# Kernel tuning notes

Measured on AMD Instinct MI355X. Metric: run time of the kernel, lower is better.

## Reference

```python
import jax, jax.numpy as jnp
import numpy as np

N, E, G, B = 50000, 1600000, 128, 128
FP = 33     # num_feature_pro
ED = 128    # embed_dim
ML = 3000   # max_len


def setup_inputs() -> dict:
    key = jax.random.key(0)
    ks = jax.random.split(key, 20)
    s = lambda k, shape: jax.random.normal(k, shape, jnp.float32) * 0.02
    inp = {}
    inp["pro_x"] = jax.random.normal(ks[0], (N, FP), jnp.float32)
    inp["edge_index"] = jax.random.randint(ks[1], (2, E), 0, N)
    inp["edge_weight"] = jax.random.uniform(ks[2], (E,), jnp.float32)
    inp["pro_batch"] = jnp.sort(jax.random.randint(ks[3], (N,), 0, G))
    inp["rna_global"] = jax.random.randint(ks[4], (B, ML), 0, 5)
    inp["rna_local"] = jax.random.randint(ks[5], (B, ML - 2), 0, 65)
    inp["emb1"] = s(ks[6], (5, ED))
    inp["emb2"] = s(ks[7], (65, ED))
    inp["convW1"] = s(ks[8], (32, ML, 8));     inp["convb1"] = jnp.zeros((32,), jnp.float32)
    inp["convW2"] = s(ks[9], (32, ML - 2, 8)); inp["convb2"] = jnp.zeros((32,), jnp.float32)
    inp["fcxr_W"] = s(ks[10], (32 * 121, 128)); inp["fcxr_b"] = jnp.zeros((128,), jnp.float32)
    inp["gcn1_W"] = s(ks[11], (FP, FP));         inp["gcn1_b"] = jnp.zeros((FP,), jnp.float32)
    inp["gcn2_W"] = s(ks[12], (FP, 2 * FP));     inp["gcn2_b"] = jnp.zeros((2 * FP,), jnp.float32)
    inp["gcn3_W"] = s(ks[13], (2 * FP, 4 * FP)); inp["gcn3_b"] = jnp.zeros((4 * FP,), jnp.float32)
    inp["bn1_g"] = jnp.ones((FP,), jnp.float32);     inp["bn1_b"] = jnp.zeros((FP,), jnp.float32)
    inp["bn2_g"] = jnp.ones((2 * FP,), jnp.float32); inp["bn2_b"] = jnp.zeros((2 * FP,), jnp.float32)
    inp["bn3_g"] = jnp.ones((4 * FP,), jnp.float32); inp["bn3_b"] = jnp.zeros((4 * FP,), jnp.float32)
    inp["fcg1_W"] = s(ks[14], (4 * FP, 1024)); inp["fcg1_b"] = jnp.zeros((1024,), jnp.float32)
    inp["fcg2_W"] = s(ks[15], (1024, 128));    inp["fcg2_b"] = jnp.zeros((128,), jnp.float32)
    return inp


def _gcn(x, W, b, src, dst, ew, n):
    # PyG GCNConv: x' = D^{-1/2}(A+I)D^{-1/2} (x W) + b, self-loop weight 1
    xw = x @ W                                           # [n, out]
    deg = jax.ops.segment_sum(ew, dst, num_segments=n) + 1.0
    dis = jax.lax.rsqrt(deg)
    norm = dis[src] * ew * dis[dst]                      # [E]
    out = jax.ops.segment_sum(xw[src] * norm[:, None], dst, num_segments=n)
    out = out + xw * (dis * dis)[:, None]                # self loops
    return out + b


def _bn(x, g, b, eps=1e-5):
    # NodeLevelBatchNorm (training): batch stats over the node dim, biased var
    m = x.mean(0)
    v = ((x - m) ** 2).mean(0)
    return (x - m) * jax.lax.rsqrt(v + eps) * g + b


def _conv1d(x, W, b):
    # x: [B, C, L], W: [O, C, K] -> [B, O, L-K+1]
    y = jax.lax.conv_general_dilated(x, W, (1,), 'VALID',
                                     dimension_numbers=('NCH', 'OIH', 'NCH'))
    return y + b[None, :, None]


def _rna(tok, emb, cW, cb, fW, fb):
    e = emb[tok]                     # [B, seq, 128] -> channels=seq, length=128
    y = _conv1d(e, cW, cb)           # [B, 32, 121]
    return y.reshape(y.shape[0], -1) @ fW + fb


def reference(pro_x, edge_index, edge_weight, pro_batch, rna_global, rna_local,
              emb1, emb2, convW1, convb1, convW2, convb2, fcxr_W, fcxr_b,
              gcn1_W, gcn1_b, gcn2_W, gcn2_b, gcn3_W, gcn3_b,
              bn1_g, bn1_b, bn2_g, bn2_b, bn3_g, bn3_b,
              fcg1_W, fcg1_b, fcg2_W, fcg2_b):
    src, dst = edge_index[0], edge_index[1]
    n = pro_x.shape[0]
    # RNA branch (fc_xr shared between global and local)
    xrg = _rna(rna_global, emb1, convW1, convb1, fcxr_W, fcxr_b)
    xrl = _rna(rna_local, emb2, convW2, convb2, fcxr_W, fcxr_b)
    # Protein GCN branch
    xp = jax.nn.relu(_bn(_gcn(pro_x, gcn1_W, gcn1_b, src, dst, edge_weight, n), bn1_g, bn1_b))
    ones = jnp.ones_like(edge_weight)
    xp = jax.nn.relu(_bn(_gcn(xp, gcn2_W, gcn2_b, src, dst, ones, n), bn2_g, bn2_b))
    xp = jax.nn.relu(_bn(_gcn(xp, gcn3_W, gcn3_b, src, dst, ones, n), bn3_g, bn3_b))
    # global mean pool per graph
    cnt = jax.ops.segment_sum(jnp.ones((n,), xp.dtype), pro_batch, num_segments=G)
    pooled = jax.ops.segment_sum(xp, pro_batch, num_segments=G) / jnp.maximum(cnt, 1.0)[:, None]
    h = jax.nn.relu(pooled @ fcg1_W + fcg1_b)
    xp_out = h @ fcg2_W + fcg2_b     # dropout = identity (eval)
    xc_rna = (xrg + xrl) * 0.5       # mean over stacked [xrg, xrl]
    return (xc_rna, xp_out)
```

## Files before the change

kernel.cpp:

```cpp
#include <hip/hip_runtime.h>
#include <hip/hip_bf16.h>

typedef __hip_bfloat16 bf16;

#define NN 50000
#define NE 1600000
#define NG 128
#define NB 128
#define SG 3000
#define SL 2998
#define VG 5
#define VL 65
#define EDB 6250
#define AGB 12500
#define NA  (NB*VG + NB*VL)
#define NGB (32*VG + 32*VL)
#define CASTB ((NN*40+255)/256)

__device__ __forceinline__ float b2f(bf16 x){ return __bfloat162float(x); }
__device__ __forceinline__ float blo(unsigned u){ return __uint_as_float(u << 16); }
__device__ __forceinline__ float bhi(unsigned u){ return __uint_as_float(u & 0xffff0000u); }

__global__ void k_front(const int* __restrict__ rna_g, const int* __restrict__ rna_l,
                        int* __restrict__ tcnt_g, int* __restrict__ toff_g,
                        int* __restrict__ bucket_g,
                        int* __restrict__ tcnt_l, int* __restrict__ toff_l,
                        int* __restrict__ bucket_l,
                        const float* __restrict__ convW1, const float* __restrict__ convW2,
                        float* __restrict__ Wr1, float* __restrict__ Wr2,
                        const float* __restrict__ fcxrW, const float* __restrict__ cb1,
                        const float* __restrict__ cb2, float* __restrict__ bias0,
                        const int* __restrict__ dst, const float* __restrict__ ew,
                        double* __restrict__ packed, int* __restrict__ slot){
    int bx = blockIdx.x;
    int t = threadIdx.x;
    if (bx < 2*NB){
        __shared__ int hist[VL], pre[VL], cur[VL];
        int br = bx & 1, b = bx >> 1;
        const int* tok = br ? rna_l : rna_g;
        int S = br ? SL : SG, V = br ? VL : VG;
        int* tcnt = br ? tcnt_l : tcnt_g;
        int* toff = br ? toff_l : toff_g;
        int* bucket = br ? bucket_l : bucket_g;
        if (t < V) hist[t] = 0;
        __syncthreads();
        for (int i = t; i < S; i += 256) atomicAdd(&hist[tok[b*S + i]], 1);
        __syncthreads();
        if (t == 0){
            int run = 0;
            for (int v = 0; v < V; ++v){ pre[v] = run; run += hist[v]; }
        }
        __syncthreads();
        if (t < V){
            tcnt[b*V + t] = hist[t];
            toff[b*V + t] = pre[t];
            cur[t] = pre[t];
        }
        __syncthreads();
        for (int i = t; i < S; i += 256){
            int v = tok[b*S + i];
            int p = atomicAdd(&cur[v], 1);
            bucket[b*S + p] = i;
        }
        return;
    }
    bx -= 2*NB;
    if (bx < EDB){
        int e = bx*256 + t;
        double old = unsafeAtomicAdd(&packed[dst[e]], 1048576.0 + (double)ew[e]);
        slot[e] = (int)(old * (1.0/1048576.0));
        return;
    }
    bx -= EDB;
    if (bx < SG + SL){
        const float* W; float* Wr; int S, c = bx;
        if (c < SG){ W = convW1; Wr = Wr1; S = SG; }
        else { c -= SG; W = convW2; Wr = Wr2; S = SL; }
        Wr[c*256 + t] = W[((t >> 3)*S + c)*8 + (t & 7)];
        return;
    }
    bx -= SG + SL;
    if (t >= 128) return;
    int o = bx, j = t;
    float s = 0.f;
    const float* Wo = fcxrW + o*121*128 + j;
    for (int l = 0; l < 121; ++l) s += Wo[l*128];
    unsafeAtomicAdd(&bias0[j], 0.5f * (cb1[o] + cb2[o]) * s);
}

__device__ void dev_buildA(const float* __restrict__ Wr, const int* __restrict__ bucket,
                           const int* __restrict__ toff, const int* __restrict__ tcnt,
                           float* __restrict__ A, int S, int V, int bv){
    int b = bv / V, v = bv - b*V;
    int t = threadIdx.x;
    const int* bk = bucket + b*S + toff[b*V + v];
    int m = tcnt[b*V + v];
    float acc = 0.f;
    int idx = 0;
    for (; idx + 4 <= m; idx += 4){
        int c0 = bk[idx], c1 = bk[idx+1], c2 = bk[idx+2], c3 = bk[idx+3];
        acc += Wr[c0*256 + t];
        acc += Wr[c1*256 + t];
        acc += Wr[c2*256 + t];
        acc += Wr[c3*256 + t];
    }
    for (; idx < m; ++idx) acc += Wr[bk[idx]*256 + t];
    A[b*(256*V) + v*256 + t] = acc;
}

__global__ void k_F1(const float* __restrict__ Wr1, const float* __restrict__ Wr2,
                     const int* __restrict__ bucket_g, const int* __restrict__ toff_g,
                     const int* __restrict__ tcnt_g, float* __restrict__ Ag,
                     const int* __restrict__ bucket_l, const int* __restrict__ toff_l,
                     const int* __restrict__ tcnt_l, float* __restrict__ Al,
                     const double* __restrict__ packed, int* __restrict__ cnt,
                     float2* __restrict__ dis12, float2* __restrict__ self12,
                     const int* __restrict__ batch, int* __restrict__ gstart,
                     int* __restrict__ bsum,
                     const float* __restrict__ fcxrb, const float* __restrict__ bias0,
                     float* __restrict__ out0){
    __shared__ int sd[256];
    int bx = blockIdx.x;
    if (bx < NA){
        if (bx < NB*VG) dev_buildA(Wr1, bucket_g, toff_g, tcnt_g, Ag, SG, VG, bx);
        else dev_buildA(Wr2, bucket_l, toff_l, tcnt_l, Al, SL, VL, bx - NB*VG);
        return;
    }
    bx -= NA;
    int t = threadIdx.x;
    if (bx == 49){
        for (int idx = t; idx < NB*128; idx += 256)
            out0[idx] = fcxrb[idx & 127] + bias0[idx & 127];
        return;
    }
    int base = bx*1024;
    int s = 0;
    #pragma unroll
    for (int j = 0; j < 4; ++j){
        int i = base + t*4 + j;
        if (i < NN){
            double p = packed[i];
            int c = (int)(p * (1.0/1048576.0));
            float w = (float)(p - (double)c * 1048576.0);
            cnt[i] = c; s += c;
            float r1 = rsqrtf(w + 1.0f);
            float r2 = rsqrtf((float)c + 1.0f);
            dis12[i] = make_float2(r1, r2);
            self12[i] = make_float2(r1*r1, r2*r2);
            int pb = batch[i];
            int prev = (i == 0) ? -1 : batch[i-1];
            for (int g = prev + 1; g <= pb; ++g) gstart[g] = i;
            if (i == NN - 1){
                for (int g = pb + 1; g <= NG; ++g) gstart[g] = NN;
            }
        }
    }
    sd[t] = s; __syncthreads();
    for (int d = 128; d > 0; d >>= 1){
        if (t < d) sd[t] += sd[t+d];
        __syncthreads();
    }
    if (t == 0) bsum[bx] = sd[0];
}

__global__ void k_scan3(const int* __restrict__ cnt, const int* __restrict__ bsum,
                        int* __restrict__ offs){
    __shared__ int sd[256];
    __shared__ int sbase;
    int t = threadIdx.x;
    if (t == 0){
        int run = 0;
        for (int i = 0; i < blockIdx.x; ++i) run += bsum[i];
        sbase = run;
    }
    int base = blockIdx.x*1024;
    int loc[4]; int s = 0;
    #pragma unroll
    for (int j = 0; j < 4; ++j){
        int idx = base + t*4 + j;
        loc[j] = (idx < NN) ? cnt[idx] : 0;
        s += loc[j];
    }
    sd[t] = s; __syncthreads();
    for (int d = 1; d < 256; d <<= 1){
        int v = (t >= d) ? sd[t-d] : 0;
        __syncthreads();
        sd[t] += v;
        __syncthreads();
    }
    int run = sbase + (sd[t] - s);
    #pragma unroll
    for (int j = 0; j < 4; ++j){
        int idx = base + t*4 + j;
        if (idx < NN) offs[idx] = run;
        run += loc[j];
    }
}

__device__ void dev_buildG(float (*rows)[128], const float* __restrict__ emb,
                           const float* __restrict__ W, bf16* __restrict__ G,
                           int V, int q){
    int o = q / V, mt = q - o*V;
    int t = threadIdx.x;
    int j = t & 127, half = t >> 7;
    int kk[4], vv[4];
    #pragma unroll
    for (int qq = 0; qq < 4; ++qq){
        int mm = half*4 + qq;
        int m = mt*8 + mm;
        int k = m / V, v = m - k*V;
        kk[qq] = k; vv[qq] = v;
        rows[mm][j] = emb[v*128 + j];
    }
    __syncthreads();
    float a0=0.f, a1=0.f, a2=0.f, a3=0.f;
    const float* Wo = W + o*121*128 + j;
    for (int l = 0; l < 121; ++l){
        float w = Wo[l*128];
        a0 += rows[half*4+0][l + kk[0]] * w;
        a1 += rows[half*4+1][l + kk[1]] * w;
        a2 += rows[half*4+2][l + kk[2]] * w;
        a3 += rows[half*4+3][l + kk[3]] * w;
    }
    float a[4] = {a0, a1, a2, a3};
    #pragma unroll
    for (int qq = 0; qq < 4; ++qq){
        int row = vv[qq]*256 + o*8 + kk[qq];
        G[(size_t)row*128 + j] = __float2bfloat16(a[qq]);
    }
}

__global__ void k_F2(const int* __restrict__ src, const int* __restrict__ dst,
                     const float* __restrict__ ew, const float2* __restrict__ dis12,
                     const int* __restrict__ offs, const int* __restrict__ slot,
                     float4* __restrict__ epk,
                     const float* __restrict__ emb1, const float* __restrict__ emb2,
                     const float* __restrict__ fcxrW, bf16* __restrict__ G1,
                     bf16* __restrict__ G2,
                     const float* __restrict__ pro_x, bf16* __restrict__ xb0){
    __shared__ float rows[8][128];
    int bx = blockIdx.x;
    if (bx < 32*VG){ dev_buildG(rows, emb1, fcxrW, G1, VG, bx); return; }
    if (bx < NGB){ dev_buildG(rows, emb2, fcxrW, G2, VL, bx - 32*VG); return; }
    bx -= NGB;
    if (bx < EDB){
        int e = bx*256 + threadIdx.x;
        int s = src[e], d = dst[e];
        int pos = offs[d] + slot[e];
        float2 a = dis12[s], b = dis12[d];
        float4 v;
        v.x = __int_as_float(s*80);
        v.y = a.x * ew[e] * b.x;
        v.z = a.y * b.y;
        v.w = __int_as_float(s*144);
        epk[pos] = v;
        return;
    }
    bx -= EDB;
    int i = bx*256 + threadIdx.x;
    if (i >= NN*40) return;
    int n = i / 40, f = i - n*40;
    xb0[i] = __float2bfloat16(f < 33 ? pro_x[n*33 + f] : 0.f);
}

template<int QV, int GRP, int OFF_W, int N_Z>
__device__ void dev_agg(float* sAgg ,
                        const bf16* __restrict__ xb, const float4* __restrict__ epk,
                        const int* __restrict__ offs, const int* __restrict__ cnt,
                        const float2* __restrict__ self12,
                        const float* __restrict__ W, const float* __restrict__ bias,
                        float* __restrict__ tout, float* __restrict__ bnpart,
                        int F, int OF, int bx){
    const int LPG = 64 / GRP;
    int wave = threadIdx.x >> 6;
    int node = bx*4 + wave;
    int lane = threadIdx.x & 63;
    int grp  = lane / LPG;
    int gl   = lane % LPG;
    bool act = gl < QV;
    const char* xc = (const char*)xb;
    float a0=0,a1=0,a2=0,a3=0,a4=0,a5=0,a6=0,a7=0;
    int b = offs[node], e = b + cnt[node];
    if (act){
        int fo = gl << 4;
        if (grp == 0){
            float2 sw2 = self12[node];
            float sw = N_Z ? sw2.y : sw2.x;
            uint4 u = *(const uint4*)(xc + node*(QV*16) + fo);
            a0 = sw*blo(u.x); a1 = sw*bhi(u.x); a2 = sw*blo(u.y); a3 = sw*bhi(u.y);
            a4 = sw*blo(u.z); a5 = sw*bhi(u.z); a6 = sw*blo(u.w); a7 = sw*bhi(u.w);
        }
        int p = b + grp;
        for (; p + 3*GRP < e; p += 4*GRP){
            float4 e0 = epk[p];
            float4 e1 = epk[p +   GRP];
            float4 e2 = epk[p + 2*GRP];
            float4 e3 = epk[p + 3*GRP];
            int o0 = __float_as_int(OFF_W ? e0.w : e0.x); float n0 = N_Z ? e0.z : e0.y;
            int o1 = __float_as_int(OFF_W ? e1.w : e1.x); float n1 = N_Z ? e1.z : e1.y;
            int o2 = __float_as_int(OFF_W ? e2.w : e2.x); float n2 = N_Z ? e2.z : e2.y;
            int o3 = __float_as_int(OFF_W ? e3.w : e3.x); float n3 = N_Z ? e3.z : e3.y;
            uint4 u0 = *(const uint4*)(xc + o0 + fo);
            uint4 u1 = *(const uint4*)(xc + o1 + fo);
            uint4 u2 = *(const uint4*)(xc + o2 + fo);
            uint4 u3 = *(const uint4*)(xc + o3 + fo);
            a0 += n0*blo(u0.x); a1 += n0*bhi(u0.x); a2 += n0*blo(u0.y); a3 += n0*bhi(u0.y);
            a4 += n0*blo(u0.z); a5 += n0*bhi(u0.z); a6 += n0*blo(u0.w); a7 += n0*bhi(u0.w);
            a0 += n1*blo(u1.x); a1 += n1*bhi(u1.x); a2 += n1*blo(u1.y); a3 += n1*bhi(u1.y);
            a4 += n1*blo(u1.z); a5 += n1*bhi(u1.z); a6 += n1*blo(u1.w); a7 += n1*bhi(u1.w);
            a0 += n2*blo(u2.x); a1 += n2*bhi(u2.x); a2 += n2*blo(u2.y); a3 += n2*bhi(u2.y);
            a4 += n2*blo(u2.z); a5 += n2*bhi(u2.z); a6 += n2*blo(u2.w); a7 += n2*bhi(u2.w);
            a0 += n3*blo(u3.x); a1 += n3*bhi(u3.x); a2 += n3*blo(u3.y); a3 += n3*bhi(u3.y);
            a4 += n3*blo(u3.z); a5 += n3*bhi(u3.z); a6 += n3*blo(u3.w); a7 += n3*bhi(u3.w);
        }
        if (p < e){
            int p1 = p + GRP, p2 = p + 2*GRP;
            bool v1 = p1 < e, v2 = p2 < e;
            float4 e0 = epk[p];
            float4 e1 = epk[v1 ? p1 : p];
            float4 e2 = epk[v2 ? p2 : p];
            int o0 = __float_as_int(OFF_W ? e0.w : e0.x);
            int o1 = __float_as_int(OFF_W ? e1.w : e1.x);
            int o2 = __float_as_int(OFF_W ? e2.w : e2.x);
            float n0 = N_Z ? e0.z : e0.y;
            float n1 = v1 ? (N_Z ? e1.z : e1.y) : 0.f;
            float n2 = v2 ? (N_Z ? e2.z : e2.y) : 0.f;
            uint4 u0 = *(const uint4*)(xc + o0 + fo);
            uint4 u1 = *(const uint4*)(xc + o1 + fo);
            uint4 u2 = *(const uint4*)(xc + o2 + fo);
            a0 += n0*blo(u0.x); a1 += n0*bhi(u0.x); a2 += n0*blo(u0.y); a3 += n0*bhi(u0.y);
            a4 += n0*blo(u0.z); a5 += n0*bhi(u0.z); a6 += n0*blo(u0.w); a7 += n0*bhi(u0.w);
            a0 += n1*blo(u1.x); a1 += n1*bhi(u1.x); a2 += n1*blo(u1.y); a3 += n1*bhi(u1.y);
            a4 += n1*blo(u1.z); a5 += n1*bhi(u1.z); a6 += n1*blo(u1.w); a7 += n1*bhi(u1.w);
            a0 += n2*blo(u2.x); a1 += n2*bhi(u2.x); a2 += n2*blo(u2.y); a3 += n2*bhi(u2.y);
            a4 += n2*blo(u2.z); a5 += n2*bhi(u2.z); a6 += n2*blo(u2.w); a7 += n2*bhi(u2.w);
        }
    }
    #pragma unroll
    for (int m = LPG; m < 64; m <<= 1){
        a0 += __shfl_xor(a0, m); a1 += __shfl_xor(a1, m);
        a2 += __shfl_xor(a2, m); a3 += __shfl_xor(a3, m);
        a4 += __shfl_xor(a4, m); a5 += __shfl_xor(a5, m);
        a6 += __shfl_xor(a6, m); a7 += __shfl_xor(a7, m);
    }
    if (act && grp == 0){
        float4* dst = (float4*)&sAgg[wave*(QV*8) + gl*8];
        dst[0] = make_float4(a0, a1, a2, a3);
        dst[1] = make_float4(a4, a5, a6, a7);
    }
    __syncthreads();
    int i0 = bx*4;
    int j = threadIdx.x;
    if (j < OF){
        float c0 = bias[j], c1 = c0, c2 = c0, c3 = c0;
        const float* Wj = W + j;
        const float* s0 = sAgg;
        const float* s1 = sAgg + QV*8;
        const float* s2 = sAgg + 2*QV*8;
        const float* s3 = sAgg + 3*QV*8;
        #pragma unroll 4
        for (int f = 0; f < F; ++f){
            float w = Wj[f*OF];
            c0 += s0[f]*w; c1 += s1[f]*w; c2 += s2[f]*w; c3 += s3[f]*w;
        }
        tout[(size_t)(i0+0)*OF + j] = c0;
        tout[(size_t)(i0+1)*OF + j] = c1;
        tout[(size_t)(i0+2)*OF + j] = c2;
        tout[(size_t)(i0+3)*OF + j] = c3;
        float s  = c0 + c1 + c2 + c3;
        float ss = c0*c0 + c1*c1 + c2*c2 + c3*c3;
        float* part = bnpart + (bx & 63)*(2*OF);
        unsafeAtomicAdd(&part[j], s);
        unsafeAtomicAdd(&part[OF + j], ss);
    }
}

template<int QV, int GRP, int OFF_W, int N_Z>
__global__ void k_agg_gemm(const bf16* __restrict__ xb, const float4* __restrict__ epk,
                           const int* __restrict__ offs, const int* __restrict__ cnt,
                           const float2* __restrict__ self12,
                           const float* __restrict__ W, const float* __restrict__ bias,
                           float* __restrict__ tout, float* __restrict__ bnpart,
                           int F, int OF){
    __shared__ float sAgg[4*QV*8];
    dev_agg<QV,GRP,OFF_W,N_Z>(sAgg, xb, epk, offs, cnt, self12, W, bias,
                              tout, bnpart, F, OF, blockIdx.x);
}

__device__ void dev_gemmR(float* xs , int bq,
                          const float* __restrict__ Ag, const bf16* __restrict__ G1,
                          const float* __restrict__ Al, const bf16* __restrict__ G2,
                          float* __restrict__ out0){
    int kpart = bq >> 4;
    int bgrp  = bq & 15;
    const float* X; const bf16* G; int K, k0;
    if (kpart < 5){ X = Ag; G = G1; K = 1280;  k0 = kpart*256; }
    else          { X = Al; G = G2; K = 16640; k0 = (kpart-5)*256; }
    int b0 = bgrp*8;
    int t = threadIdx.x;
    #pragma unroll
    for (int i = 0; i < 8; ++i)
        xs[i*256 + t] = X[(b0+i)*K + k0 + t];
    __syncthreads();
    int rq = t >> 7, j = t & 127;
    const float* x0 = xs + (rq*4)*256;
    float a0=0,a1=0,a2=0,a3=0;
    const bf16* Gp = G + (size_t)k0*128 + j;
    for (int kk = 0; kk < 256; ++kk){
        float g = b2f(Gp[kk*128]);
        a0 += x0[kk]*g; a1 += x0[256+kk]*g; a2 += x0[512+kk]*g; a3 += x0[768+kk]*g;
    }
    unsafeAtomicAdd(&out0[(b0+rq*4+0)*128 + j], 0.5f*a0);
    unsafeAtomicAdd(&out0[(b0+rq*4+1)*128 + j], 0.5f*a1);
    unsafeAtomicAdd(&out0[(b0+rq*4+2)*128 + j], 0.5f*a2);
    unsafeAtomicAdd(&out0[(b0+rq*4+3)*128 + j], 0.5f*a3);
}

__global__ void k_L3(const bf16* __restrict__ xb, const float4* __restrict__ epk,
                     const int* __restrict__ offs, const int* __restrict__ cnt,
                     const float2* __restrict__ self12,
                     const float* __restrict__ W, const float* __restrict__ bias,
                     float* __restrict__ tout, float* __restrict__ bnpart,
                     const float* __restrict__ Ag, const bf16* __restrict__ G1,
                     const float* __restrict__ Al, const bf16* __restrict__ G2,
                     float* __restrict__ out0){
    __shared__ float smem[8*256];
    int bx = blockIdx.x;
    if (bx < AGB){
        dev_agg<9,4,1,1>(smem, xb, epk, offs, cnt, self12, W, bias, tout, bnpart,
                         66, 132, bx);
    } else {
        dev_gemmR(smem, bx - AGB, Ag, G1, Al, G2, out0);
    }
}

__global__ void k_bn_fin(const float* __restrict__ part, float* __restrict__ sums, int OF){
    int tid = threadIdx.x;
    if (tid >= 2*OF) return;
    float s = 0.f;
    #pragma unroll 8
    for (int k = 0; k < 64; ++k) s += part[k*(2*OF) + tid];
    sums[tid] = s;
}

__global__ void k_bn_apply(const float* __restrict__ t, const float* __restrict__ sums,
                           const float* __restrict__ g, const float* __restrict__ b,
                           bf16* __restrict__ xo, int OF, int OS, int total){
    int id = blockIdx.x*256 + threadIdx.x;
    if (id >= total) return;
    int i = id / OS, f = id - i*OS;
    float v = 0.f;
    if (f < OF){
        float m  = sums[f] * (1.0f/(float)NN);
        float vr = sums[OF + f] * (1.0f/(float)NN) - m*m;
        float sc = g[f] * rsqrtf(vr + 1e-5f);
        float sh = b[f] - m*sc;
        v = t[(size_t)i*OF + f] * sc + sh;
        v = v > 0.f ? v : 0.f;
    }
    xo[id] = __float2bfloat16(v);
}

__global__ void k_poolBN(const float* __restrict__ t, const float* __restrict__ sums,
                         const float* __restrict__ g, const float* __restrict__ b,
                         const int* __restrict__ gstart, float* __restrict__ poolsum){
    int gr = blockIdx.x, strip = blockIdx.y, f = threadIdx.x;
    if (f >= 132) return;
    float m  = sums[f] * (1.0f/(float)NN);
    float vr = sums[132 + f] * (1.0f/(float)NN) - m*m;
    float sc = g[f] * rsqrtf(vr + 1e-5f);
    float sh = b[f] - m*sc;
    int i0 = gstart[gr], i1 = gstart[gr+1];
    float s = 0.f;
    for (int i = i0 + strip; i < i1; i += 4){
        float v = t[(size_t)i*132 + f] * sc + sh;
        s += v > 0.f ? v : 0.f;
    }
    unsafeAtomicAdd(&poolsum[gr*132 + f], s);
}

__global__ void k_fcgF(const float* __restrict__ poolsum, const int* __restrict__ gstart,
                       const float* __restrict__ W1, const float* __restrict__ b1,
                       const float* __restrict__ W2, const float* __restrict__ b2,
                       float* __restrict__ out){
    __shared__ float pr[132];
    __shared__ float hr[1024];
    __shared__ float part[8][128];
    int g = blockIdx.x, t = threadIdx.x;
    if (t < 132){
        float inv = 1.0f / fmaxf((float)(gstart[g+1] - gstart[g]), 1.0f);
        pr[t] = poolsum[g*132 + t] * inv;
    }
    __syncthreads();
    float acc = b1[t];
    #pragma unroll 4
    for (int f = 0; f < 132; ++f) acc += pr[f] * W1[f*1024 + t];
    hr[t] = acc > 0.f ? acc : 0.f;
    __syncthreads();
    int ks = t >> 7, j = t & 127;
    const float* Wp = W2 + (ks*128)*128 + j;
    const float* hp = hr + ks*128;
    float a = 0.f;
    #pragma unroll 8
    for (int kk = 0; kk < 128; ++kk) a += hp[kk] * Wp[(size_t)kk*128];
    part[ks][j] = a;
    __syncthreads();
    if (t < 128){
        float s = b2[t];
        #pragma unroll
        for (int r = 0; r < 8; ++r) s += part[r][t];
        out[g*128 + t] = s;
    }
}

extern "C" void kernel_launch(void* const* d_in, const int* in_sizes, int n_in,
                              void* d_out, int out_size, void* d_ws, size_t ws_size,
                              hipStream_t stream)
{
    (void)in_sizes; (void)n_in; (void)out_size; (void)ws_size;

    const float* pro_x  = (const float*)d_in[0];
    const int*   eidx   = (const int*)  d_in[1];
    const float* ew     = (const float*)d_in[2];
    const int*   pbatch = (const int*)  d_in[3];
    const int*   rna_g  = (const int*)  d_in[4];
    const int*   rna_l  = (const int*)  d_in[5];
    const float* emb1   = (const float*)d_in[6];
    const float* emb2   = (const float*)d_in[7];
    const float* convW1 = (const float*)d_in[8];
    const float* convb1 = (const float*)d_in[9];
    const float* convW2 = (const float*)d_in[10];
    const float* convb2 = (const float*)d_in[11];
    const float* fcxrW  = (const float*)d_in[12];
    const float* fcxrb  = (const float*)d_in[13];
    const float* g1W = (const float*)d_in[14];
    const float* g1b = (const float*)d_in[15];
    const float* g2W = (const float*)d_in[16];
    const float* g2b = (const float*)d_in[17];
    const float* g3W = (const float*)d_in[18];
    const float* g3b = (const float*)d_in[19];
    const float* bn1g = (const float*)d_in[20];
    const float* bn1b = (const float*)d_in[21];
    const float* bn2g = (const float*)d_in[22];
    const float* bn2b = (const float*)d_in[23];
    const float* bn3g = (const float*)d_in[24];
    const float* bn3b = (const float*)d_in[25];
    const float* fcg1W = (const float*)d_in[26];
    const float* fcg1b = (const float*)d_in[27];
    const float* fcg2W = (const float*)d_in[28];
    const float* fcg2b = (const float*)d_in[29];

    const int* e_src = eidx;
    const int* e_dst = eidx + NE;

    char* base = (char*)d_ws;
    size_t off = 0;
    auto alloc = [&](size_t bytes)->char*{
        off = (off + 255) & ~(size_t)255;
        char* p = base + off; off += bytes; return p;
    };

    double* packed  = (double*)alloc(NN*8);
    float* bnsum1  = (float*)alloc(2*33*4);
    float* bnsum2  = (float*)alloc(2*66*4);
    float* bnsum3  = (float*)alloc(2*132*4);
    float* poolsum = (float*)alloc(NG*132*4);
    float* bias0   = (float*)alloc(128*4);
    float* bnpart1 = (float*)alloc(64*2*33*4);
    float* bnpart2 = (float*)alloc(64*2*66*4);
    float* bnpart3 = (float*)alloc(64*2*132*4);
    size_t zero_bytes = (off + 255) & ~(size_t)255;

    int*    cnt    = (int*)   alloc(NN*4);
    float2* dis12  = (float2*)alloc(NN*8);
    float2* self12 = (float2*)alloc(NN*8);
    int*    offs   = (int*)   alloc(NN*4);
    int*    bsum   = (int*)   alloc(64*4);
    int*    gstart = (int*)   alloc((NG+1)*4);
    float4* epk    = (float4*)alloc((size_t)NE*16);
    float*  bufB   = (float*) alloc((size_t)NN*132*4);
    bf16*   xbA    = (bf16*)  alloc((size_t)NE*4);
    bf16*   xbB    = (bf16*)  alloc((size_t)NN*72*2);
    float*  Ag     = (float*) alloc((size_t)NB*256*VG*4);
    float*  Al     = (float*) alloc((size_t)NB*256*VL*4);
    bf16*   G1     = (bf16*)  alloc((size_t)32*8*VG*128*2);
    bf16*   G2     = (bf16*)  alloc((size_t)32*8*VL*128*2);

    int*  slot = (int*)xbA;
    bf16* xb0  = (bf16*)xbB;

    float* out0 = (float*)d_out;
    float* out1 = (float*)d_out + 16384;

    char* rb = (char*)bufB;
    size_t ro = 0;
    auto ralloc = [&](size_t bytes)->char*{
        ro = (ro + 255) & ~(size_t)255;
        char* p = rb + ro; ro += bytes; return p;
    };
    int* toff_g   = (int*)ralloc(NB*VG*4);
    int* toff_l   = (int*)ralloc(NB*VL*4);
    int* tcnt_g   = (int*)ralloc(NB*VG*4);
    int* tcnt_l   = (int*)ralloc(NB*VL*4);
    int* bucket_g = (int*)ralloc((size_t)NB*SG*4);
    int* bucket_l = (int*)ralloc((size_t)NB*SL*4);
    float* Wr1    = (float*)ralloc((size_t)SG*256*4);
    float* Wr2    = (float*)ralloc((size_t)SL*256*4);

    hipMemsetAsync(d_ws, 0, zero_bytes, stream);

    k_front<<<2*NB + EDB + SG + SL + 32, 256, 0, stream>>>(
        rna_g, rna_l, tcnt_g, toff_g, bucket_g, tcnt_l, toff_l, bucket_l,
        convW1, convW2, Wr1, Wr2, fcxrW, convb1, convb2, bias0,
        e_dst, ew, packed, slot);

    k_F1<<<NA + 50, 256, 0, stream>>>(Wr1, Wr2,
                                      bucket_g, toff_g, tcnt_g, Ag,
                                      bucket_l, toff_l, tcnt_l, Al,
                                      packed, cnt, dis12, self12, pbatch, gstart,
                                      bsum, fcxrb, bias0, out0);
    k_scan3<<<49, 256, 0, stream>>>(cnt, bsum, offs);

    k_F2<<<NGB + EDB + CASTB, 256, 0, stream>>>(
        e_src, e_dst, ew, dis12, offs, slot, epk,
        emb1, emb2, fcxrW, G1, G2, pro_x, xb0);

    k_agg_gemm<5,8,0,0><<<AGB, 256, 0, stream>>>(xb0, epk, offs, cnt, self12,
                                                 g1W, g1b, bufB, bnpart1, 33, 33);
    k_bn_fin<<<1, 512, 0, stream>>>(bnpart1, bnsum1, 33);
    k_bn_apply<<<(NN*40+255)/256, 256, 0, stream>>>(bufB, bnsum1, bn1g, bn1b,
                                                    xbA, 33, 40, NN*40);

    k_agg_gemm<5,8,0,1><<<AGB, 256, 0, stream>>>(xbA, epk, offs, cnt, self12,
                                                 g2W, g2b, bufB, bnpart2, 33, 66);
    k_bn_fin<<<1, 512, 0, stream>>>(bnpart2, bnsum2, 66);
    k_bn_apply<<<(NN*72+255)/256, 256, 0, stream>>>(bufB, bnsum2, bn2g, bn2b,
                                                    xbB, 66, 72, NN*72);

    k_L3<<<AGB + 1120, 256, 0, stream>>>(xbB, epk, offs, cnt, self12,
                                         g3W, g3b, bufB, bnpart3, Ag, G1, Al, G2, out0);
    k_bn_fin<<<1, 512, 0, stream>>>(bnpart3, bnsum3, 132);

    k_poolBN<<<dim3(NG,4), 192, 0, stream>>>(bufB, bnsum3, bn3g, bn3b, gstart, poolsum);
    k_fcgF<<<NG, 1024, 0, stream>>>(poolsum, gstart, fcg1W, fcg1b, fcg2W, fcg2b, out1);
}
```

Before: 571.5 us.

## Remap GCN gather lanes to power-of-two slots with tail chunk handled by lane zero

Restructures the edge-gather aggregation so each wave splits into 64/MAIN edge slots of MAIN lanes (4 or 8) instead of groups with idle lanes (QV=5 or 9 in groups of 8 or 16 lanes). The leftover 16-byte feature chunk per row is handled by lane 0 of each slot with a second accumulator set. This packs more edges per wave and removes masked-off lanes. It also lowers unroll depth from 4 to 2 and adds launch bounds for 8 blocks per CU. The extra divergent lane-0 loads and doubled shuffle reductions add cost and create load imbalance within each slot.

Result: slower. 604.6 us (+5.8%).

```diff
diff --git a/kernel.cpp b/kernel.cpp
--- a/kernel.cpp
+++ b/kernel.cpp
@@ -263,7 +263,7 @@
     xb0[i] = __float2bfloat16(f < 33 ? pro_x[n*33 + f] : 0.f);
 }
 
-template<int QV, int GRP, int OFF_W, int N_Z>
+template<int MAIN, int OFF_W, int N_Z>
 __device__ void dev_agg(float* sAgg ,
                         const bf16* __restrict__ xb, const float4* __restrict__ epk,
                         const int* __restrict__ offs, const int* __restrict__ cnt,
@@ -271,82 +271,86 @@
                         const float* __restrict__ W, const float* __restrict__ bias,
                         float* __restrict__ tout, float* __restrict__ bnpart,
                         int F, int OF, int bx){
-    const int LPG = 64 / GRP;
+    const int NS  = 64 / MAIN;
+    const int ROW = (MAIN + 1) * 16;
+    const int PW  = (MAIN + 1) * 8;
     int wave = threadIdx.x >> 6;
     int node = bx*4 + wave;
     int lane = threadIdx.x & 63;
-    int grp  = lane / LPG;
-    int gl   = lane % LPG;
-    bool act = gl < QV;
+    int slot = lane / MAIN;
+    int gl   = lane & (MAIN - 1);
     const char* xc = (const char*)xb;
+    int fo = gl << 4;
+    const int fe = MAIN << 4;
     float a0=0,a1=0,a2=0,a3=0,a4=0,a5=0,a6=0,a7=0;
-    int b = offs[node], e = b + cnt[node];
-    if (act){
-        int fo = gl << 4;
-        if (grp == 0){
-            float2 sw2 = self12[node];
-            float sw = N_Z ? sw2.y : sw2.x;
-            uint4 u = *(const uint4*)(xc + node*(QV*16) + fo);
-            a0 = sw*blo(u.x); a1 = sw*bhi(u.x); a2 = sw*blo(u.y); a3 = sw*bhi(u.y);
-            a4 = sw*blo(u.z); a5 = sw*bhi(u.z); a6 = sw*blo(u.w); a7 = sw*bhi(u.w);
-        }
-        int p = b + grp;
-        for (; p + 3*GRP < e; p += 4*GRP){
-            float4 e0 = epk[p];
-            float4 e1 = epk[p +   GRP];
-            float4 e2 = epk[p + 2*GRP];
-            float4 e3 = epk[p + 3*GRP];
-            int o0 = __float_as_int(OFF_W ? e0.w : e0.x); float n0 = N_Z ? e0.z : e0.y;
-            int o1 = __float_as_int(OFF_W ? e1.w : e1.x); float n1 = N_Z ? e1.z : e1.y;
-            int o2 = __float_as_int(OFF_W ? e2.w : e2.x); float n2 = N_Z ? e2.z : e2.y;
-            int o3 = __float_as_int(OFF_W ? e3.w : e3.x); float n3 = N_Z ? e3.z : e3.y;
-            uint4 u0 = *(const uint4*)(xc + o0 + fo);
-            uint4 u1 = *(const uint4*)(xc + o1 + fo);
-            uint4 u2 = *(const uint4*)(xc + o2 + fo);
-            uint4 u3 = *(const uint4*)(xc + o3 + fo);
-            a0 += n0*blo(u0.x); a1 += n0*bhi(u0.x); a2 += n0*blo(u0.y); a3 += n0*bhi(u0.y);
-            a4 += n0*blo(u0.z); a5 += n0*bhi(u0.z); a6 += n0*blo(u0.w); a7 += n0*bhi(u0.w);
-            a0 += n1*blo(u1.x); a1 += n1*bhi(u1.x); a2 += n1*blo(u1.y); a3 += n1*bhi(u1.y);
-            a4 += n1*blo(u1.z); a5 += n1*bhi(u1.z); a6 += n1*blo(u1.w); a7 += n1*bhi(u1.w);
-            a0 += n2*blo(u2.x); a1 += n2*bhi(u2.x); a2 += n2*blo(u2.y); a3 += n2*bhi(u2.y);
-            a4 += n2*blo(u2.z); a5 += n2*bhi(u2.z); a6 += n2*blo(u2.w); a7 += n2*bhi(u2.w);
-            a0 += n3*blo(u3.x); a1 += n3*bhi(u3.x); a2 += n3*blo(u3.y); a3 += n3*bhi(u3.y);
-            a4 += n3*blo(u3.z); a5 += n3*bhi(u3.z); a6 += n3*blo(u3.w); a7 += n3*bhi(u3.w);
-        }
-        if (p < e){
-            int p1 = p + GRP, p2 = p + 2*GRP;
-            bool v1 = p1 < e, v2 = p2 < e;
-            float4 e0 = epk[p];
-            float4 e1 = epk[v1 ? p1 : p];
-            float4 e2 = epk[v2 ? p2 : p];
-            int o0 = __float_as_int(OFF_W ? e0.w : e0.x);
-            int o1 = __float_as_int(OFF_W ? e1.w : e1.x);
-            int o2 = __float_as_int(OFF_W ? e2.w : e2.x);
-            float n0 = N_Z ? e0.z : e0.y;
-            float n1 = v1 ? (N_Z ? e1.z : e1.y) : 0.f;
-            float n2 = v2 ? (N_Z ? e2.z : e2.y) : 0.f;
-            uint4 u0 = *(const uint4*)(xc + o0 + fo);
-            uint4 u1 = *(const uint4*)(xc + o1 + fo);
-            uint4 u2 = *(const uint4*)(xc + o2 + fo);
-            a0 += n0*blo(u0.x); a1 += n0*bhi(u0.x); a2 += n0*blo(u0.y); a3 += n0*bhi(u0.y);
-            a4 += n0*blo(u0.z); a5 += n0*bhi(u0.z); a6 += n0*blo(u0.w); a7 += n0*bhi(u0.w);
-            a0 += n1*blo(u1.x); a1 += n1*bhi(u1.x); a2 += n1*blo(u1.y); a3 += n1*bhi(u1.y);
-            a4 += n1*blo(u1.z); a5 += n1*bhi(u1.z); a6 += n1*blo(u1.w); a7 += n1*bhi(u1.w);
-            a0 += n2*blo(u2.x); a1 += n2*bhi(u2.x); a2 += n2*blo(u2.y); a3 += n2*bhi(u2.y);
-            a4 += n2*blo(u2.z); a5 += n2*bhi(u2.z); a6 += n2*blo(u2.w); a7 += n2*bhi(u2.w);
+    float b0=0,b1=0,b2=0,b3=0,b4=0,b5=0,b6=0,b7=0;
+    int bg = offs[node], e = bg + cnt[node];
+    if (slot == 0){
+        float2 sw2 = self12[node];
+        float sw = N_Z ? sw2.y : sw2.x;
+        const char* rp = xc + (size_t)node*ROW;
+        uint4 u = *(const uint4*)(rp + fo);
+        a0 = sw*blo(u.x); a1 = sw*bhi(u.x); a2 = sw*blo(u.y); a3 = sw*bhi(u.y);
+        a4 = sw*blo(u.z); a5 = sw*bhi(u.z); a6 = sw*blo(u.w); a7 = sw*bhi(u.w);
+        if (gl == 0){
+            uint4 v = *(const uint4*)(rp + fe);
+            b0 = sw*blo(v.x); b1 = sw*bhi(v.x); b2 = sw*blo(v.y); b3 = sw*bhi(v.y);
+            b4 = sw*blo(v.z); b5 = sw*bhi(v.z); b6 = sw*blo(v.w); b7 = sw*bhi(v.w);
+        }
+    }
+    int p = bg + slot;
+    for (; p + NS < e; p += 2*NS){
+        float4 e0 = epk[p];
+        float4 e1 = epk[p + NS];
+        int o0 = __float_as_int(OFF_W ? e0.w : e0.x); float n0 = N_Z ? e0.z : e0.y;
+        int o1 = __float_as_int(OFF_W ? e1.w : e1.x); float n1 = N_Z ? e1.z : e1.y;
+        uint4 u0 = *(const uint4*)(xc + o0 + fo);
+        uint4 u1 = *(const uint4*)(xc + o1 + fo);
+        a0 += n0*blo(u0.x); a1 += n0*bhi(u0.x); a2 += n0*blo(u0.y); a3 += n0*bhi(u0.y);
+        a4 += n0*blo(u0.z); a5 += n0*bhi(u0.z); a6 += n0*blo(u0.w); a7 += n0*bhi(u0.w);
+        a0 += n1*blo(u1.x); a1 += n1*bhi(u1.x); a2 += n1*blo(u1.y); a3 += n1*bhi(u1.y);
+        a4 += n1*blo(u1.z); a5 += n1*bhi(u1.z); a6 += n1*blo(u1.w); a7 += n1*bhi(u1.w);
+        if (gl == 0){
+            uint4 v0 = *(const uint4*)(xc + o0 + fe);
+            uint4 v1 = *(const uint4*)(xc + o1 + fe);
+            b0 += n0*blo(v0.x); b1 += n0*bhi(v0.x); b2 += n0*blo(v0.y); b3 += n0*bhi(v0.y);
+            b4 += n0*blo(v0.z); b5 += n0*bhi(v0.z); b6 += n0*blo(v0.w); b7 += n0*bhi(v0.w);
+            b0 += n1*blo(v1.x); b1 += n1*bhi(v1.x); b2 += n1*blo(v1.y); b3 += n1*bhi(v1.y);
+            b4 += n1*blo(v1.z); b5 += n1*bhi(v1.z); b6 += n1*blo(v1.w); b7 += n1*bhi(v1.w);
+        }
+    }
+    if (p < e){
+        float4 e0 = epk[p];
+        int o0 = __float_as_int(OFF_W ? e0.w : e0.x); float n0 = N_Z ? e0.z : e0.y;
+        uint4 u0 = *(const uint4*)(xc + o0 + fo);
+        a0 += n0*blo(u0.x); a1 += n0*bhi(u0.x); a2 += n0*blo(u0.y); a3 += n0*bhi(u0.y);
+        a4 += n0*blo(u0.z); a5 += n0*bhi(u0.z); a6 += n0*blo(u0.w); a7 += n0*bhi(u0.w);
+        if (gl == 0){
+            uint4 v0 = *(const uint4*)(xc + o0 + fe);
+            b0 += n0*blo(v0.x); b1 += n0*bhi(v0.x); b2 += n0*blo(v0.y); b3 += n0*bhi(v0.y);
+            b4 += n0*blo(v0.z); b5 += n0*bhi(v0.z); b6 += n0*blo(v0.w); b7 += n0*bhi(v0.w);
         }
     }
     #pragma unroll
-    for (int m = LPG; m < 64; m <<= 1){
+    for (int m = MAIN; m < 64; m <<= 1){
         a0 += __shfl_xor(a0, m); a1 += __shfl_xor(a1, m);
         a2 += __shfl_xor(a2, m); a3 += __shfl_xor(a3, m);
         a4 += __shfl_xor(a4, m); a5 += __shfl_xor(a5, m);
         a6 += __shfl_xor(a6, m); a7 += __shfl_xor(a7, m);
-    }
-    if (act && grp == 0){
-        float4* dst = (float4*)&sAgg[wave*(QV*8) + gl*8];
-        dst[0] = make_float4(a0, a1, a2, a3);
-        dst[1] = make_float4(a4, a5, a6, a7);
+        b0 += __shfl_xor(b0, m); b1 += __shfl_xor(b1, m);
+        b2 += __shfl_xor(b2, m); b3 += __shfl_xor(b3, m);
+        b4 += __shfl_xor(b4, m); b5 += __shfl_xor(b5, m);
+        b6 += __shfl_xor(b6, m); b7 += __shfl_xor(b7, m);
+    }
+    if (slot == 0){
+        float4* d = (float4*)&sAgg[wave*PW + gl*8];
+        d[0] = make_float4(a0, a1, a2, a3);
+        d[1] = make_float4(a4, a5, a6, a7);
+        if (gl == 0){
+            float4* d2 = (float4*)&sAgg[wave*PW + MAIN*8];
+            d2[0] = make_float4(b0, b1, b2, b3);
+            d2[1] = make_float4(b4, b5, b6, b7);
+        }
     }
     __syncthreads();
     int i0 = bx*4;
@@ -355,9 +359,9 @@
         float c0 = bias[j], c1 = c0, c2 = c0, c3 = c0;
         const float* Wj = W + j;
         const float* s0 = sAgg;
-        const float* s1 = sAgg + QV*8;
-        const float* s2 = sAgg + 2*QV*8;
-        const float* s3 = sAgg + 3*QV*8;
+        const float* s1 = sAgg + PW;
+        const float* s2 = sAgg + 2*PW;
+        const float* s3 = sAgg + 3*PW;
         #pragma unroll 4
         for (int f = 0; f < F; ++f){
             float w = Wj[f*OF];
@@ -375,16 +379,17 @@
     }
 }
 
-template<int QV, int GRP, int OFF_W, int N_Z>
-__global__ void k_agg_gemm(const bf16* __restrict__ xb, const float4* __restrict__ epk,
-                           const int* __restrict__ offs, const int* __restrict__ cnt,
-                           const float2* __restrict__ self12,
-                           const float* __restrict__ W, const float* __restrict__ bias,
-                           float* __restrict__ tout, float* __restrict__ bnpart,
-                           int F, int OF){
-    __shared__ float sAgg[4*QV*8];
-    dev_agg<QV,GRP,OFF_W,N_Z>(sAgg, xb, epk, offs, cnt, self12, W, bias,
-                              tout, bnpart, F, OF, blockIdx.x);
+template<int MAIN, int OFF_W, int N_Z>
+__global__ __launch_bounds__(256, 8)
+void k_agg_gemm(const bf16* __restrict__ xb, const float4* __restrict__ epk,
+                const int* __restrict__ offs, const int* __restrict__ cnt,
+                const float2* __restrict__ self12,
+                const float* __restrict__ W, const float* __restrict__ bias,
+                float* __restrict__ tout, float* __restrict__ bnpart,
+                int F, int OF){
+    __shared__ float sAgg[4*(MAIN+1)*8];
+    dev_agg<MAIN,OFF_W,N_Z>(sAgg, xb, epk, offs, cnt, self12, W, bias,
+                            tout, bnpart, F, OF, blockIdx.x);
 }
 
 __device__ void dev_gemmR(float* xs , int bq,
@@ -416,19 +421,20 @@
     unsafeAtomicAdd(&out0[(b0+rq*4+3)*128 + j], 0.5f*a3);
 }
 
-__global__ void k_L3(const bf16* __restrict__ xb, const float4* __restrict__ epk,
-                     const int* __restrict__ offs, const int* __restrict__ cnt,
-                     const float2* __restrict__ self12,
-                     const float* __restrict__ W, const float* __restrict__ bias,
-                     float* __restrict__ tout, float* __restrict__ bnpart,
-                     const float* __restrict__ Ag, const bf16* __restrict__ G1,
-                     const float* __restrict__ Al, const bf16* __restrict__ G2,
-                     float* __restrict__ out0){
+__global__ __launch_bounds__(256, 8)
+void k_L3(const bf16* __restrict__ xb, const float4* __restrict__ epk,
+          const int* __restrict__ offs, const int* __restrict__ cnt,
+          const float2* __restrict__ self12,
+          const float* __restrict__ W, const float* __restrict__ bias,
+          float* __restrict__ tout, float* __restrict__ bnpart,
+          const float* __restrict__ Ag, const bf16* __restrict__ G1,
+          const float* __restrict__ Al, const bf16* __restrict__ G2,
+          float* __restrict__ out0){
     __shared__ float smem[8*256];
     int bx = blockIdx.x;
     if (bx < AGB){
-        dev_agg<9,4,1,1>(smem, xb, epk, offs, cnt, self12, W, bias, tout, bnpart,
-                         66, 132, bx);
+        dev_agg<8,1,1>(smem, xb, epk, offs, cnt, self12, W, bias, tout, bnpart,
+                       66, 132, bx);
     } else {
         dev_gemmR(smem, bx - AGB, Ag, G1, Al, G2, out0);
     }
@@ -625,14 +631,14 @@
         e_src, e_dst, ew, dis12, offs, slot, epk,
         emb1, emb2, fcxrW, G1, G2, pro_x, xb0);
 
-    k_agg_gemm<5,8,0,0><<<AGB, 256, 0, stream>>>(xb0, epk, offs, cnt, self12,
-                                                 g1W, g1b, bufB, bnpart1, 33, 33);
+    k_agg_gemm<4,0,0><<<AGB, 256, 0, stream>>>(xb0, epk, offs, cnt, self12,
+                                               g1W, g1b, bufB, bnpart1, 33, 33);
     k_bn_fin<<<1, 512, 0, stream>>>(bnpart1, bnsum1, 33);
     k_bn_apply<<<(NN*40+255)/256, 256, 0, stream>>>(bufB, bnsum1, bn1g, bn1b,
                                                     xbA, 33, 40, NN*40);
 
-    k_agg_gemm<5,8,0,1><<<AGB, 256, 0, stream>>>(xbA, epk, offs, cnt, self12,
-                                                 g2W, g2b, bufB, bnpart2, 33, 66);
+    k_agg_gemm<4,0,1><<<AGB, 256, 0, stream>>>(xbA, epk, offs, cnt, self12,
+                                               g2W, g2b, bufB, bnpart2, 33, 66);
     k_bn_fin<<<1, 512, 0, stream>>>(bnpart2, bnsum2, 66);
     k_bn_apply<<<(NN*72+255)/256, 256, 0, stream>>>(bufB, bnsum2, bn2g, bn2b,
                                                     xbB, 66, 72, NN*72);
```

## Move RNA A-matrix build into first GCN aggregation kernel and shrink buckets to u16

Applied to the files above, without the earlier changes.

The RNA token-bucket accumulation (buildA) moves out of the small prep kernel and into the first GCN aggregation launch, so the two independent workloads share one grid and run concurrently. The prep kernel becomes a 50-block launch that only does the degree and normalisation work, which shortens the serial path before the edge packing. Bucket indices shrink from int to u16 to halve that traffic, and the RNA scratch buffers move to dedicated workspace instead of aliasing bufB, which the layer-1 output now overwrites. Launch bounds are added to the aggregation kernels, which may constrain register allocation.

Result: slower. 590.8 us (+3.4%).

```diff
diff --git a/kernel.cpp b/kernel.cpp
--- a/kernel.cpp
+++ b/kernel.cpp
@@ -2,6 +2,7 @@
 #include <hip/hip_bf16.h>
 
 typedef __hip_bfloat16 bf16;
+typedef unsigned short u16;
 
 #define NN 50000
 #define NE 1600000
@@ -23,9 +24,9 @@
 
 __global__ void k_front(const int* __restrict__ rna_g, const int* __restrict__ rna_l,
                         int* __restrict__ tcnt_g, int* __restrict__ toff_g,
-                        int* __restrict__ bucket_g,
+                        u16* __restrict__ bucket_g,
                         int* __restrict__ tcnt_l, int* __restrict__ toff_l,
-                        int* __restrict__ bucket_l,
+                        u16* __restrict__ bucket_l,
                         const float* __restrict__ convW1, const float* __restrict__ convW2,
                         float* __restrict__ Wr1, float* __restrict__ Wr2,
                         const float* __restrict__ fcxrW, const float* __restrict__ cb1,
@@ -41,7 +42,7 @@
         int S = br ? SL : SG, V = br ? VL : VG;
         int* tcnt = br ? tcnt_l : tcnt_g;
         int* toff = br ? toff_l : toff_g;
-        int* bucket = br ? bucket_l : bucket_g;
+        u16* bucket = br ? bucket_l : bucket_g;
         if (t < V) hist[t] = 0;
         __syncthreads();
         for (int i = t; i < S; i += 256) atomicAdd(&hist[tok[b*S + i]], 1);
@@ -60,7 +61,7 @@
         for (int i = t; i < S; i += 256){
             int v = tok[b*S + i];
             int p = atomicAdd(&cur[v], 1);
-            bucket[b*S + p] = i;
+            bucket[b*S + p] = (u16)i;
         }
         return;
     }
@@ -88,12 +89,12 @@
     unsafeAtomicAdd(&bias0[j], 0.5f * (cb1[o] + cb2[o]) * s);
 }
 
-__device__ void dev_buildA(const float* __restrict__ Wr, const int* __restrict__ bucket,
+__device__ void dev_buildA(const float* __restrict__ Wr, const u16* __restrict__ bucket,
                            const int* __restrict__ toff, const int* __restrict__ tcnt,
                            float* __restrict__ A, int S, int V, int bv){
     int b = bv / V, v = bv - b*V;
     int t = threadIdx.x;
-    const int* bk = bucket + b*S + toff[b*V + v];
+    const u16* bk = bucket + b*S + toff[b*V + v];
     int m = tcnt[b*V + v];
     float acc = 0.f;
     int idx = 0;
@@ -108,32 +109,20 @@
     A[b*(256*V) + v*256 + t] = acc;
 }
 
-__global__ void k_F1(const float* __restrict__ Wr1, const float* __restrict__ Wr2,
-                     const int* __restrict__ bucket_g, const int* __restrict__ toff_g,
-                     const int* __restrict__ tcnt_g, float* __restrict__ Ag,
-                     const int* __restrict__ bucket_l, const int* __restrict__ toff_l,
-                     const int* __restrict__ tcnt_l, float* __restrict__ Al,
-                     const double* __restrict__ packed, int* __restrict__ cnt,
-                     float2* __restrict__ dis12, float2* __restrict__ self12,
-                     const int* __restrict__ batch, int* __restrict__ gstart,
-                     int* __restrict__ bsum,
-                     const float* __restrict__ fcxrb, const float* __restrict__ bias0,
-                     float* __restrict__ out0){
+__global__ void k_prep(const double* __restrict__ packed, int* __restrict__ cnt,
+                       float2* __restrict__ dis12, float2* __restrict__ self12,
+                       const int* __restrict__ batch, int* __restrict__ gstart,
+                       int* __restrict__ bsum,
+                       const float* __restrict__ fcxrb, const float* __restrict__ bias0,
+                       float* __restrict__ out0){
     __shared__ int sd[256];
-    int bx = blockIdx.x;
-    if (bx < NA){
-        if (bx < NB*VG) dev_buildA(Wr1, bucket_g, toff_g, tcnt_g, Ag, SG, VG, bx);
-        else dev_buildA(Wr2, bucket_l, toff_l, tcnt_l, Al, SL, VL, bx - NB*VG);
-        return;
-    }
-    bx -= NA;
     int t = threadIdx.x;
-    if (bx == 49){
+    if (blockIdx.x == 49){
         for (int idx = t; idx < NB*128; idx += 256)
             out0[idx] = fcxrb[idx & 127] + bias0[idx & 127];
         return;
     }
-    int base = bx*1024;
+    int base = blockIdx.x*1024;
     int s = 0;
     #pragma unroll
     for (int j = 0; j < 4; ++j){
@@ -160,7 +149,7 @@
         if (t < d) sd[t] += sd[t+d];
         __syncthreads();
     }
-    if (t == 0) bsum[bx] = sd[0];
+    if (t == 0) bsum[blockIdx.x] = sd[0];
 }
 
 __global__ void k_scan3(const int* __restrict__ cnt, const int* __restrict__ bsum,
@@ -375,13 +364,36 @@
     }
 }
 
+__global__ __launch_bounds__(256, 8)
+void k_L1(const float* __restrict__ Wr1, const float* __restrict__ Wr2,
+          const u16* __restrict__ bucket_g, const int* __restrict__ toff_g,
+          const int* __restrict__ tcnt_g, float* __restrict__ Ag,
+          const u16* __restrict__ bucket_l, const int* __restrict__ toff_l,
+          const int* __restrict__ tcnt_l, float* __restrict__ Al,
+          const bf16* __restrict__ xb, const float4* __restrict__ epk,
+          const int* __restrict__ offs, const int* __restrict__ cnt,
+          const float2* __restrict__ self12,
+          const float* __restrict__ W, const float* __restrict__ bias,
+          float* __restrict__ tout, float* __restrict__ bnpart){
+    __shared__ float sAgg[4*5*8];
+    int bx = blockIdx.x;
+    if (bx < NA){
+        if (bx < NB*VG) dev_buildA(Wr1, bucket_g, toff_g, tcnt_g, Ag, SG, VG, bx);
+        else dev_buildA(Wr2, bucket_l, toff_l, tcnt_l, Al, SL, VL, bx - NB*VG);
+        return;
+    }
+    dev_agg<5,8,0,0>(sAgg, xb, epk, offs, cnt, self12, W, bias,
+                     tout, bnpart, 33, 33, bx - NA);
+}
+
 template<int QV, int GRP, int OFF_W, int N_Z>
-__global__ void k_agg_gemm(const bf16* __restrict__ xb, const float4* __restrict__ epk,
-                           const int* __restrict__ offs, const int* __restrict__ cnt,
-                           const float2* __restrict__ self12,
-                           const float* __restrict__ W, const float* __restrict__ bias,
-                           float* __restrict__ tout, float* __restrict__ bnpart,
-                           int F, int OF){
+__global__ __launch_bounds__(256, 8)
+void k_agg_gemm(const bf16* __restrict__ xb, const float4* __restrict__ epk,
+                const int* __restrict__ offs, const int* __restrict__ cnt,
+                const float2* __restrict__ self12,
+                const float* __restrict__ W, const float* __restrict__ bias,
+                float* __restrict__ tout, float* __restrict__ bnpart,
+                int F, int OF){
     __shared__ float sAgg[4*QV*8];
     dev_agg<QV,GRP,OFF_W,N_Z>(sAgg, xb, epk, offs, cnt, self12, W, bias,
                               tout, bnpart, F, OF, blockIdx.x);
@@ -585,27 +597,20 @@
     float*  Al     = (float*) alloc((size_t)NB*256*VL*4);
     bf16*   G1     = (bf16*)  alloc((size_t)32*8*VG*128*2);
     bf16*   G2     = (bf16*)  alloc((size_t)32*8*VL*128*2);
+    int* toff_g   = (int*)alloc(NB*VG*4);
+    int* toff_l   = (int*)alloc(NB*VL*4);
+    int* tcnt_g   = (int*)alloc(NB*VG*4);
+    int* tcnt_l   = (int*)alloc(NB*VL*4);
+    u16* bucket_g = (u16*)alloc((size_t)NB*SG*2);
+    u16* bucket_l = (u16*)alloc((size_t)NB*SL*2);
+    float* Wr1    = (float*)alloc((size_t)SG*256*4);
+    float* Wr2    = (float*)alloc((size_t)SL*256*4);
 
     int*  slot = (int*)xbA;
     bf16* xb0  = (bf16*)xbB;
 
     float* out0 = (float*)d_out;
     float* out1 = (float*)d_out + 16384;
-
-    char* rb = (char*)bufB;
-    size_t ro = 0;
-    auto ralloc = [&](size_t bytes)->char*{
-        ro = (ro + 255) & ~(size_t)255;
-        char* p = rb + ro; ro += bytes; return p;
-    };
-    int* toff_g   = (int*)ralloc(NB*VG*4);
-    int* toff_l   = (int*)ralloc(NB*VL*4);
-    int* tcnt_g   = (int*)ralloc(NB*VG*4);
-    int* tcnt_l   = (int*)ralloc(NB*VL*4);
-    int* bucket_g = (int*)ralloc((size_t)NB*SG*4);
-    int* bucket_l = (int*)ralloc((size_t)NB*SL*4);
-    float* Wr1    = (float*)ralloc((size_t)SG*256*4);
-    float* Wr2    = (float*)ralloc((size_t)SL*256*4);
 
     hipMemsetAsync(d_ws, 0, zero_bytes, stream);
 
@@ -614,19 +619,19 @@
         convW1, convW2, Wr1, Wr2, fcxrW, convb1, convb2, bias0,
         e_dst, ew, packed, slot);
 
-    k_F1<<<NA + 50, 256, 0, stream>>>(Wr1, Wr2,
-                                      bucket_g, toff_g, tcnt_g, Ag,
-                                      bucket_l, toff_l, tcnt_l, Al,
-                                      packed, cnt, dis12, self12, pbatch, gstart,
-                                      bsum, fcxrb, bias0, out0);
+    k_prep<<<50, 256, 0, stream>>>(packed, cnt, dis12, self12, pbatch, gstart,
+                                   bsum, fcxrb, bias0, out0);
     k_scan3<<<49, 256, 0, stream>>>(cnt, bsum, offs);
 
     k_F2<<<NGB + EDB + CASTB, 256, 0, stream>>>(
         e_src, e_dst, ew, dis12, offs, slot, epk,
         emb1, emb2, fcxrW, G1, G2, pro_x, xb0);
 
-    k_agg_gemm<5,8,0,0><<<AGB, 256, 0, stream>>>(xb0, epk, offs, cnt, self12,
-                                                 g1W, g1b, bufB, bnpart1, 33, 33);
+    k_L1<<<NA + AGB, 256, 0, stream>>>(Wr1, Wr2,
+                                       bucket_g, toff_g, tcnt_g, Ag,
+                                       bucket_l, toff_l, tcnt_l, Al,
+                                       xb0, epk, offs, cnt, self12,
+                                       g1W, g1b, bufB, bnpart1);
     k_bn_fin<<<1, 512, 0, stream>>>(bnpart1, bnsum1, 33);
     k_bn_apply<<<(NN*40+255)/256, 256, 0, stream>>>(bufB, bnsum1, bn1g, bn1b,
                                                     xbA, 33, 40, NN*40);
```
